# Kernel optimization log

Hardware: AMD Instinct MI355X
Metric: run time of the kernel (lower is better)

## Reference

```python
import jax, jax.numpy as jnp
import numpy as np

N = 50000      # nodes
E = 400000     # directed edges (self-loops added inside reference, per PyG default)
DIN = 256
DH = 32
HEADS = 8
DOUT = 40
SLOPE = 0.2    # GATv2Conv negative_slope default


def _gatv2_layer(x, src, dst, Wl, bl, Wr, br, att, bias, heads, out_ch):
    """One GATv2Conv (concat=True). x:[n,din], src/dst:[e], att:[heads,out_ch]."""
    n = x.shape[0]
    xl = (x @ Wl + bl).reshape(n, heads, out_ch)   # source transform
    xr = (x @ Wr + br).reshape(n, heads, out_ch)   # target transform
    e = jax.nn.leaky_relu(xl[src] + xr[dst], SLOPE)          # [e, H, C]
    s = jnp.einsum('ehc,hc->eh', e, att)                     # per-edge attention logits
    smax = jax.ops.segment_max(s, dst, num_segments=n)       # stable softmax over in-edges
    ex = jnp.exp(s - smax[dst])
    denom = jax.ops.segment_sum(ex, dst, num_segments=n)
    alpha = ex / denom[dst]                                  # [e, H]
    out = jax.ops.segment_sum(alpha[:, :, None] * xl[src], dst, num_segments=n)
    return out.reshape(n, heads * out_ch) + bias


def setup_inputs() -> dict:
    key = jax.random.key(0)
    ks = jax.random.split(key, 8)
    def gl(k, shape, fan_in):
        return jax.random.normal(k, shape, jnp.float32) * np.float32(1.0 / np.sqrt(fan_in))
    return {
        'x': jax.random.normal(ks[0], (N, DIN), jnp.float32),
        'edge_index': jax.random.randint(ks[1], (2, E), 0, N, jnp.int32),
        'W1l': gl(ks[2], (DIN, HEADS * DH), DIN),
        'b1l': jnp.zeros((HEADS * DH,), jnp.float32),
        'W1r': gl(ks[3], (DIN, HEADS * DH), DIN),
        'b1r': jnp.zeros((HEADS * DH,), jnp.float32),
        'att1': gl(ks[4], (HEADS, DH), DH),
        'bias1': jnp.zeros((HEADS * DH,), jnp.float32),
        'W2l': gl(ks[5], (HEADS * DH, DOUT), HEADS * DH),
        'b2l': jnp.zeros((DOUT,), jnp.float32),
        'W2r': gl(ks[6], (HEADS * DH, DOUT), HEADS * DH),
        'b2r': jnp.zeros((DOUT,), jnp.float32),
        'att2': gl(ks[7], (1, DOUT), DOUT),
        'bias2': jnp.zeros((DOUT,), jnp.float32),
    }


def reference(x, edge_index, W1l, b1l, W1r, b1r, att1, bias1,
              W2l, b2l, W2r, b2r, att2, bias2):
    n = x.shape[0]
    loop = jnp.arange(n, dtype=edge_index.dtype)  # add_self_loops=True (PyG default)
    src = jnp.concatenate([edge_index[0], loop])
    dst = jnp.concatenate([edge_index[1], loop])
    # eval mode: F.dropout is identity; normalization='none' -> Identity
    h = _gatv2_layer(x, src, dst, W1l, b1l, W1r, b1r, att1, bias1, HEADS, DH)
    h = jax.nn.elu(h)
    out = _gatv2_layer(h, src, dst, W2l, b2l, W2r, b2r, att2, bias2, 1, DOUT)
    return jax.nn.log_softmax(out, axis=1)
```

## Files before the change

### kernel.cpp

```cpp
#include <hip/hip_runtime.h>
#include <math.h>

#define NODES 50000
#define NEDGE 400000
#define ETOT  450000
#define DIN   256
#define C1    256
#define C2    40
#define SCAN_NB ((NODES + 255) / 256)
#define CSRCAP  600064
#define NB_CNT ((ETOT + 255) / 256)
#define NB_CVT (NODES * DIN / 8 / 256)

typedef __attribute__((ext_vector_type(8))) short bfrag;
typedef __attribute__((ext_vector_type(4))) float facc;

#define GPTR(p) (const __attribute__((address_space(1))) unsigned int*)(p)
#define LPTR(p) (__attribute__((address_space(3))) unsigned int*)(p)

static __device__ __forceinline__ float bitsf(unsigned int x) {
    float f;
    __builtin_memcpy(&f, &x, 4);
    return f;
}
static __device__ __forceinline__ unsigned short f2bf(float f) {
    unsigned int x;
    __builtin_memcpy(&x, &f, 4);
    unsigned int r = x + 0x7fffu + ((x >> 16) & 1u);
    return (unsigned short)(r >> 16);
}
static __device__ __forceinline__ float fexp2(float x) {
#if __has_builtin(__builtin_amdgcn_exp2f)
    return __builtin_amdgcn_exp2f(x);
#else
    return exp2f(x);
#endif
}

__global__ __launch_bounds__(256)
void prep_a(const int* __restrict__ dstRow, int* __restrict__ cnt,
            const float* __restrict__ x, unsigned short* __restrict__ xb)
{
    if (blockIdx.x < NB_CNT) {
        int e = blockIdx.x * 256 + threadIdx.x;
        if (e >= ETOT) return;
        int d = (e < NEDGE) ? dstRow[e] : (e - NEDGE);
        atomicAdd(&cnt[d], 1);
    } else {
        int i = (blockIdx.x - NB_CNT) * 256 + threadIdx.x;
        const float4* p = (const float4*)x + (size_t)i * 2;
        float4 u0 = p[0], u1 = p[1];
        bfrag pk;
        pk[0] = (short)f2bf(u0.x); pk[1] = (short)f2bf(u0.y);
        pk[2] = (short)f2bf(u0.z); pk[3] = (short)f2bf(u0.w);
        pk[4] = (short)f2bf(u1.x); pk[5] = (short)f2bf(u1.y);
        pk[6] = (short)f2bf(u1.z); pk[7] = (short)f2bf(u1.w);
        *(bfrag*)(xb + (size_t)i * 8) = pk;
    }
}

__global__ __launch_bounds__(256)
void prep_ww(const float* __restrict__ W1l, const float* __restrict__ W1r,
             unsigned short* __restrict__ Wt1,
             const float* __restrict__ W2l, const float* __restrict__ W2r,
             unsigned short* __restrict__ Wt2)
{
    if (blockIdx.x < 512) {
        const int idx = blockIdx.x * 256 + threadIdx.x;
        const int n = idx >> 8;
        const int k = idx & 255;
        float v = (n < C1) ? W1l[(size_t)k * C1 + n] : W1r[(size_t)k * C1 + (n - C1)];
        Wt1[idx] = f2bf(v);
    } else {
        const int idx = (blockIdx.x - 512) * 256 + threadIdx.x;
        const int n = idx >> 8;
        const int k = idx & 255;
        if (n >= 2 * C2) return;
        float v = (n < C2) ? W2l[(size_t)k * C2 + n] : W2r[(size_t)k * C2 + (n - C2)];
        Wt2[idx] = f2bf(v);
    }
}

__global__ __launch_bounds__(256)
void scan_blk(const int* __restrict__ cnt, int* __restrict__ off, int* __restrict__ blkTot) {
    __shared__ int buf[256];
    const int t = threadIdx.x;
    const int i = blockIdx.x * 256 + t;
    int v = (i < NODES) ? ((cnt[i] + 3) & ~3) : 0;
    buf[t] = v;
    __syncthreads();
    #pragma unroll
    for (int d = 1; d < 256; d <<= 1) {
        int add = (t >= d) ? buf[t - d] : 0;
        __syncthreads();
        buf[t] += add;
        __syncthreads();
    }
    if (i < NODES) off[i] = buf[t] - v;
    if (t == 255) blkTot[blockIdx.x] = buf[255];
}

__global__ __launch_bounds__(256)
void scan_top(const int* __restrict__ blkTot, int* __restrict__ blkOff, int* __restrict__ offEnd) {
    __shared__ int buf[256];
    const int t = threadIdx.x;
    int v = (t < SCAN_NB) ? blkTot[t] : 0;
    buf[t] = v;
    __syncthreads();
    #pragma unroll
    for (int d = 1; d < 256; d <<= 1) {
        int add = (t >= d) ? buf[t - d] : 0;
        __syncthreads();
        buf[t] += add;
        __syncthreads();
    }
    if (t < SCAN_NB) blkOff[t] = buf[t] - v;
    if (t == 255) *offEnd = buf[255];
}

__global__ __launch_bounds__(256)
void scan_fix(int* __restrict__ off, int* __restrict__ wrk, const int* __restrict__ blkOff) {
    const int i = blockIdx.x * 256 + threadIdx.x;
    if (i < NODES) {
        int v = off[i] + blkOff[blockIdx.x];
        off[i] = v;
        wrk[i] = v;
    }
}

__global__ void place_kernel(const int* __restrict__ srcRow, const int* __restrict__ dstRow,
                             int* __restrict__ wrk, int* __restrict__ csr) {
    int e = blockIdx.x * blockDim.x + threadIdx.x;
    if (e >= ETOT) return;
    int d, s;
    if (e < NEDGE) { d = dstRow[e]; s = srcRow[e]; }
    else           { d = e - NEDGE; s = d; }
    int slot = atomicAdd(&wrk[d], 1);
    csr[slot] = s;
}

#define GBM 128
#define GBN 128
#define GBK 32

template<typename OUTT, bool SWZ>
__global__ __launch_bounds__(256)
void mfma_gemm(const unsigned short* __restrict__ Ab, const unsigned short* __restrict__ Bt,
               const float* __restrict__ bl, const float* __restrict__ br,
               OUTT* __restrict__ Cl, OUTT* __restrict__ Cr,
               int M, int Nrows, int Nhalf, int nbnShift)
{
    __shared__ __align__(16) unsigned short As[3][GBM * GBK];
    __shared__ __align__(16) unsigned short Bs[3][GBN * GBK];

    const int tid  = threadIdx.x;
    const int lane = tid & 63;
    const int w    = tid >> 6;
    const int wr   = w >> 1;
    const int wc   = w & 1;

    int tile;
    if constexpr (SWZ) {
        const int nwg = gridDim.x;
        const int q = nwg >> 3, r = nwg & 7;
        const int xcd = blockIdx.x & 7;
        const int idx = blockIdx.x >> 3;
        tile = (xcd < r ? xcd * (q + 1) : r * (q + 1) + (xcd - r) * q) + idx;
    } else {
        tile = blockIdx.x;
    }
    const int bx   = tile >> nbnShift;
    const int by   = tile & ((1 << nbnShift) - 1);
    const int row0 = bx * GBM;
    const int col0 = by * GBN;

    facc acc[4][4];
    #pragma unroll
    for (int i = 0; i < 4; ++i)
        #pragma unroll
        for (int j = 0; j < 4; ++j) {
            facc z = {0.f, 0.f, 0.f, 0.f};
            acc[i][j] = z;
        }

    const int rA  = lane >> 2;
    const int kgA = (lane & 3) ^ ((rA >> 1) & 3);
    const int fr    = lane & 15;
    const int sRead = (lane >> 4) ^ ((fr >> 1) & 3);

    #define STAGE(bufi, k0)                                                     \
    {                                                                           \
        _Pragma("unroll")                                                       \
        for (int p = 0; p < 2; ++p) {                                           \
            const int chunk = p * 4 + w;                                        \
            const int r_loc = chunk * 16 + rA;                                  \
            const int ga = min(row0 + r_loc, M - 1);                            \
            __builtin_amdgcn_global_load_lds(                                   \
                GPTR(Ab + (size_t)ga * 256 + (k0) + kgA * 8),                   \
                LPTR(&As[bufi][chunk * 512]), 16, 0, 0);                        \
            const int gb = min(col0 + r_loc, Nrows - 1);                        \
            __builtin_amdgcn_global_load_lds(                                   \
                GPTR(Bt + (size_t)gb * 256 + (k0) + kgA * 8),                   \
                LPTR(&Bs[bufi][chunk * 512]), 16, 0, 0);                        \
        }                                                                       \
    }

    #define KSTEP(T, WSTR)                                                      \
    {                                                                           \
        asm volatile("s_waitcnt vmcnt(" WSTR ")" ::: "memory");                 \
        __builtin_amdgcn_s_barrier();                                           \
        __builtin_amdgcn_sched_barrier(0);                                      \
        constexpr int cur = (T) % 3;                                            \
        bfrag af[4], bfv[4];                                                    \
        _Pragma("unroll")                                                       \
        for (int mi = 0; mi < 4; ++mi)                                          \
            af[mi] = *(const bfrag*)(&As[cur][(wr * 64 + mi * 16 + fr) * 32 + sRead * 8]); \
        _Pragma("unroll")                                                       \
        for (int ni = 0; ni < 4; ++ni)                                          \
            bfv[ni] = *(const bfrag*)(&Bs[cur][(wc * 64 + ni * 16 + fr) * 32 + sRead * 8]); \
        if constexpr ((T) + 2 < 8) STAGE(((T) + 2) % 3, ((T) + 2) * GBK);       \
        _Pragma("unroll")                                                       \
        for (int mi = 0; mi < 4; ++mi)                                          \
            _Pragma("unroll")                                                   \
            for (int ni = 0; ni < 4; ++ni)                                      \
                acc[mi][ni] = __builtin_amdgcn_mfma_f32_16x16x32_bf16(          \
                    af[mi], bfv[ni], acc[mi][ni], 0, 0, 0);                     \
    }

    STAGE(0, 0 * GBK);
    STAGE(1, 1 * GBK);
    KSTEP(0, "4"); KSTEP(1, "4"); KSTEP(2, "4"); KSTEP(3, "4");
    KSTEP(4, "4"); KSTEP(5, "4"); KSTEP(6, "4"); KSTEP(7, "0");
    #undef KSTEP
    #undef STAGE

    #pragma unroll
    for (int mi = 0; mi < 4; ++mi) {
        const int rbase = row0 + wr * 64 + mi * 16 + ((lane >> 4) << 2);
        #pragma unroll
        for (int ni = 0; ni < 4; ++ni) {
            const int col = col0 + wc * 64 + ni * 16 + (lane & 15);
            #pragma unroll
            for (int rg = 0; rg < 4; ++rg) {
                int r = rbase + rg;
                if (r >= M) continue;
                float v = acc[mi][ni][rg];
                if (col < Nhalf) {
                    v += bl[col];
                    if constexpr (sizeof(OUTT) == 2)
                        Cl[(size_t)r * Nhalf + col] = (OUTT)f2bf(v);
                    else
                        Cl[(size_t)r * Nhalf + col] = (OUTT)v;
                } else if (col < 2 * Nhalf) {
                    int c2 = col - Nhalf;
                    v += br[c2];
                    if constexpr (sizeof(OUTT) == 2)
                        Cr[(size_t)r * Nhalf + c2] = (OUTT)f2bf(v);
                    else
                        Cr[(size_t)r * Nhalf + c2] = (OUTT)v;
                }
            }
        }
    }
}

__global__ __launch_bounds__(256)
void fused_l1(const int* __restrict__ off, const int* __restrict__ deg,
              const int* __restrict__ csr, const unsigned short* __restrict__ xl,
              const unsigned short* __restrict__ xr, const float* __restrict__ att,
              const float* __restrict__ bias, unsigned short* __restrict__ hout)
{
    const int lane = threadIdx.x & 63;
    const int n    = blockIdx.x * 4 + (threadIdx.x >> 6);
    if (n >= NODES) return;

    const int a  = __builtin_amdgcn_readfirstlane(off[n]);
    const int dn = __builtin_amdgcn_readfirstlane(deg[n]);
    const int np = (dn + 3) & ~3;

    const uint2 xrn = *(const uint2*)(xr + (size_t)n * C1 + lane * 4);
    const float xr0 = bitsf(xrn.x << 16), xr1 = bitsf(xrn.x & 0xffff0000u);
    const float xr2 = bitsf(xrn.y << 16), xr3 = bitsf(xrn.y & 0xffff0000u);
    const float4 wv = *(const float4*)(att + lane * 4);
    const float L2E = 1.4426950408889634f;
    const float w6_0 = wv.x * (0.6f * L2E), w4_0 = wv.x * (0.4f * L2E);
    const float w6_1 = wv.y * (0.6f * L2E), w4_1 = wv.y * (0.4f * L2E);
    const float w6_2 = wv.z * (0.6f * L2E), w4_2 = wv.z * (0.4f * L2E);
    const float w6_3 = wv.w * (0.6f * L2E), w4_3 = wv.w * (0.4f * L2E);

    float m = -INFINITY, d = 0.f;
    float a0 = 0.f, a1 = 0.f, a2 = 0.f, a3 = 0.f;

    uint2 R[4];
    {
        const int4 s4 = *(const int4*)(csr + a);
        R[0] = *(const uint2*)(xl + (size_t)s4.x * C1 + lane * 4);
        R[1] = *(const uint2*)(xl + (size_t)s4.y * C1 + lane * 4);
        R[2] = *(const uint2*)(xl + (size_t)s4.z * C1 + lane * 4);
        R[3] = *(const uint2*)(xl + (size_t)s4.w * C1 + lane * 4);
    }

    for (int i = 0; i < np; i += 4) {
        uint2 Rn[4];
        const int nx = (i + 4 < np) ? (i + 4) : i;
        {
            const int4 s4 = *(const int4*)(csr + a + nx);
            Rn[0] = *(const uint2*)(xl + (size_t)s4.x * C1 + lane * 4);
            Rn[1] = *(const uint2*)(xl + (size_t)s4.y * C1 + lane * 4);
            Rn[2] = *(const uint2*)(xl + (size_t)s4.z * C1 + lane * 4);
            Rn[3] = *(const uint2*)(xl + (size_t)s4.w * C1 + lane * 4);
        }

        float x0[4], x1[4], x2[4], x3[4], p[4];
        #pragma unroll
        for (int k = 0; k < 4; ++k) {
            x0[k] = bitsf(R[k].x << 16);
            x1[k] = bitsf(R[k].x & 0xffff0000u);
            x2[k] = bitsf(R[k].y << 16);
            x3[k] = bitsf(R[k].y & 0xffff0000u);
            const float v0 = x0[k] + xr0, v1 = x1[k] + xr1;
            const float v2 = x2[k] + xr2, v3 = x3[k] + xr3;
            float pp;
            pp = w6_0 * v0;
            pp = fmaf(w4_0, fabsf(v0), pp);
            pp = fmaf(w6_1, v1, pp);
            pp = fmaf(w4_1, fabsf(v1), pp);
            pp = fmaf(w6_2, v2, pp);
            pp = fmaf(w4_2, fabsf(v2), pp);
            pp = fmaf(w6_3, v3, pp);
            pp = fmaf(w4_3, fabsf(v3), pp);
            pp += __shfl_xor(pp, 1);
            pp += __shfl_xor(pp, 2);
            pp += __shfl_xor(pp, 4);
            p[k] = (i + k < dn) ? pp : -INFINITY;
        }

        const float pm = fmaxf(fmaxf(p[0], p[1]), fmaxf(p[2], p[3]));
        if (__any(pm > m + 8.f)) {
            #pragma unroll
            for (int k = 0; k < 4; ++k) {
                const float mN = fmaxf(m, p[k]);
                const float sc = fexp2(m - mN);
                const float wg = fexp2(p[k] - mN);
                m = mN;
                d = fmaf(d, sc, wg);
                a0 = fmaf(wg, x0[k], a0 * sc);
                a1 = fmaf(wg, x1[k], a1 * sc);
                a2 = fmaf(wg, x2[k], a2 * sc);
                a3 = fmaf(wg, x3[k], a3 * sc);
            }
        } else {
            #pragma unroll
            for (int k = 0; k < 4; ++k) {
                const float wg = fexp2(p[k] - m);
                d += wg;
                a0 = fmaf(wg, x0[k], a0);
                a1 = fmaf(wg, x1[k], a1);
                a2 = fmaf(wg, x2[k], a2);
                a3 = fmaf(wg, x3[k], a3);
            }
        }

        #pragma unroll
        for (int k = 0; k < 4; ++k) R[k] = Rn[k];
    }

    const float inv = 1.f / d;
    const float4 bv = *(const float4*)(bias + lane * 4);
    float v0 = fmaf(a0, inv, bv.x), v1 = fmaf(a1, inv, bv.y);
    float v2 = fmaf(a2, inv, bv.z), v3 = fmaf(a3, inv, bv.w);
    v0 = v0 > 0.f ? v0 : (fexp2(v0 * L2E) - 1.f);
    v1 = v1 > 0.f ? v1 : (fexp2(v1 * L2E) - 1.f);
    v2 = v2 > 0.f ? v2 : (fexp2(v2 * L2E) - 1.f);
    v3 = v3 > 0.f ? v3 : (fexp2(v3 * L2E) - 1.f);
    uint2 o;
    o.x = (unsigned int)f2bf(v0) | ((unsigned int)f2bf(v1) << 16);
    o.y = (unsigned int)f2bf(v2) | ((unsigned int)f2bf(v3) << 16);
    *(uint2*)(hout + (size_t)n * C1 + lane * 4) = o;
}

__global__ __launch_bounds__(256)
void fused_l2(const int* __restrict__ off, const int* __restrict__ deg,
              const int* __restrict__ csr, const float* __restrict__ h2l,
              const float* __restrict__ h2r, const float* __restrict__ att,
              const float* __restrict__ bias, float* __restrict__ out)
{
    const int lane = threadIdx.x & 63;
    const int n    = blockIdx.x * 4 + (threadIdx.x >> 6);
    if (n >= NODES) return;
    const int l8 = lane & 7;
    const int g  = lane >> 3;

    const int a  = __builtin_amdgcn_readfirstlane(off[n]);
    const int dn = __builtin_amdgcn_readfirstlane(deg[n]);
    const float L2E = 1.4426950408889634f;

    float w6[5], w4[5], xr[5];
    #pragma unroll
    for (int j = 0; j < 5; ++j) {
        const int c = l8 + 8 * j;
        const float w = att[c];
        w6[j] = w * (0.6f * L2E);
        w4[j] = w * (0.4f * L2E);
        xr[j] = h2r[(size_t)n * C2 + c];
    }

    float m = -INFINITY, dl = 0.f;
    float acc[5] = {0.f, 0.f, 0.f, 0.f, 0.f};

    float R[5];
    {
        const int src = csr[a + g];
        const float* row = h2l + (size_t)src * C2 + l8;
        #pragma unroll
        for (int j = 0; j < 5; ++j) R[j] = row[8 * j];
    }

    for (int c0 = 0; c0 < dn; c0 += 8) {
        float Rn[5];
        {
            const int nx = (c0 + 8 < dn) ? (c0 + 8) : c0;
            const int src = csr[a + nx + g];
            const float* row = h2l + (size_t)src * C2 + l8;
            #pragma unroll
            for (int j = 0; j < 5; ++j) Rn[j] = row[8 * j];
        }

        const int idx = c0 + g;
        float p = 0.f;
        #pragma unroll
        for (int j = 0; j < 5; ++j) {
            const float v = R[j] + xr[j];
            p = fmaf(w6[j], v, p);
            p = fmaf(w4[j], fabsf(v), p);
        }
        p += __shfl_xor(p, 1);
        p += __shfl_xor(p, 2);
        p += __shfl_xor(p, 4);
        if (idx >= dn) p = -INFINITY;

        if (__any(p > m + 8.f)) {
            float pm = p;
            pm = fmaxf(pm, __shfl_xor(pm, 8));
            pm = fmaxf(pm, __shfl_xor(pm, 16));
            pm = fmaxf(pm, __shfl_xor(pm, 32));
            const float mN = fmaxf(m, pm);
            const float sc = fexp2(m - mN);
            const float wg = fexp2(p - mN);
            m = mN;
            dl = fmaf(dl, sc, wg);
            #pragma unroll
            for (int j = 0; j < 5; ++j) acc[j] = fmaf(wg, R[j], acc[j] * sc);
        } else {
            const float wg = fexp2(p - m);
            dl += wg;
            #pragma unroll
            for (int j = 0; j < 5; ++j) acc[j] = fmaf(wg, R[j], acc[j]);
        }

        #pragma unroll
        for (int j = 0; j < 5; ++j) R[j] = Rn[j];
    }

    #pragma unroll
    for (int o = 8; o < 64; o <<= 1) {
        dl += __shfl_xor(dl, o);
        #pragma unroll
        for (int j = 0; j < 5; ++j) acc[j] += __shfl_xor(acc[j], o);
    }

    const float inv = 1.f / dl;
    float v[5];
    float mx = -INFINITY;
    #pragma unroll
    for (int j = 0; j < 5; ++j) {
        v[j] = fmaf(acc[j], inv, bias[l8 + 8 * j]);
        mx = fmaxf(mx, v[j]);
    }
    mx = fmaxf(mx, __shfl_xor(mx, 1));
    mx = fmaxf(mx, __shfl_xor(mx, 2));
    mx = fmaxf(mx, __shfl_xor(mx, 4));
    float s = 0.f;
    #pragma unroll
    for (int j = 0; j < 5; ++j) s += fexp2((v[j] - mx) * L2E);
    s += __shfl_xor(s, 1);
    s += __shfl_xor(s, 2);
    s += __shfl_xor(s, 4);
    const float lg = logf(s);
    if (g == 0) {
        #pragma unroll
        for (int j = 0; j < 5; ++j)
            out[(size_t)n * C2 + l8 + 8 * j] = v[j] - mx - lg;
    }
}

extern "C" void kernel_launch(void* const* d_in, const int* in_sizes, int n_in,
                              void* d_out, int out_size, void* d_ws, size_t ws_size,
                              hipStream_t stream)
{
    const float* x     = (const float*)d_in[0];
    const int*   ei    = (const int*)  d_in[1];
    const float* W1l   = (const float*)d_in[2];
    const float* b1l   = (const float*)d_in[3];
    const float* W1r   = (const float*)d_in[4];
    const float* b1r   = (const float*)d_in[5];
    const float* att1  = (const float*)d_in[6];
    const float* bias1 = (const float*)d_in[7];
    const float* W2l   = (const float*)d_in[8];
    const float* b2l   = (const float*)d_in[9];
    const float* W2r   = (const float*)d_in[10];
    const float* b2r   = (const float*)d_in[11];
    const float* att2  = (const float*)d_in[12];
    const float* bias2 = (const float*)d_in[13];
    float* out = (float*)d_out;

    float* ws = (float*)d_ws;
    unsigned short* xl1 = (unsigned short*)ws;
    unsigned short* xr1 = (unsigned short*)(ws + 6400000);
    unsigned short* xb  = (unsigned short*)(ws + 12800000);
    int*   csr    = (int*)(ws + 19200000);
    int*   off    = csr + CSRCAP;
    int*   cnt    = off + (NODES + 1);
    int*   wrk    = cnt + NODES;
    int*   blkTot = wrk + NODES;
    int*   blkOff = blkTot + SCAN_NB;
    unsigned short* Wt1 = (unsigned short*)(ws + 19960000);
    unsigned short* Wt2 = (unsigned short*)(ws + 20030000);
    unsigned short* h = xr1;
    float* h2l = ws;
    float* h2r = ws + 2000000;

    const int* srcRow = ei;
    const int* dstRow = ei + NEDGE;

    hipMemsetAsync(cnt, 0, NODES * sizeof(int), stream);
    hipMemsetAsync(csr, 0, CSRCAP * sizeof(int), stream);
    prep_a<<<NB_CNT + NB_CVT, 256, 0, stream>>>(dstRow, cnt, x, xb);
    prep_ww<<<512 + 80, 256, 0, stream>>>(W1l, W1r, Wt1, W2l, W2r, Wt2);

    scan_blk<<<SCAN_NB, 256, 0, stream>>>(cnt, off, blkTot);
    scan_top<<<1, 256, 0, stream>>>(blkTot, blkOff, off + NODES);
    scan_fix<<<SCAN_NB, 256, 0, stream>>>(off, wrk, blkOff);
    place_kernel<<<(ETOT + 255) / 256, 256, 0, stream>>>(srcRow, dstRow, wrk, csr);

    mfma_gemm<unsigned short, true><<<((NODES + GBM - 1) / GBM) * 4, 256, 0, stream>>>(
        xb, Wt1, b1l, b1r, xl1, xr1, NODES, 2 * C1, C1, 2);
    fused_l1<<<(NODES + 3) / 4, 256, 0, stream>>>(off, cnt, csr, xl1, xr1, att1, bias1, h);

    mfma_gemm<float, false><<<(NODES + GBM - 1) / GBM, 256, 0, stream>>>(
        h, Wt2, b2l, b2r, h2l, h2r, NODES, 2 * C2, C2, 0);
    fused_l2<<<(NODES + 3) / 4, 256, 0, stream>>>(off, cnt, csr, h2l, h2r, att2, bias2, out);
}
```

Before: 204.3 us.

## Add 128x256-tile, 512-thread GEMM for layer-1 projection with XCD-aware remap

Replaces the generic 128x128 MFMA GEMM for the layer-1 projection (x @ [Wl|Wr]) with a dedicated kernel. It uses 128x256 tiles, 8 waves, double-buffered direct global-to-LDS loads and a fully unrolled K loop. Block indices are remapped so neighbouring tiles land on the same XCD, and larger tiles mean fewer re-reads of the A matrix. The cost is higher LDS and register use per block, which can lower occupancy, and only two buffers are kept where the old kernel used three.

After: 214.4 us. 4.9% more time.

```diff
diff --git a/kernel.cpp b/kernel.cpp
--- a/kernel.cpp
+++ b/kernel.cpp
@@ -137,6 +137,118 @@
     else           { d = e - NEDGE; s = d; }
     int slot = atomicAdd(&wrk[d], 1);
     csr[slot] = s;
+}
+
+__global__ __launch_bounds__(512)
+void gemm1_big(const unsigned short* __restrict__ Ab, const unsigned short* __restrict__ Bt,
+               const float* __restrict__ bl, const float* __restrict__ br,
+               unsigned short* __restrict__ Cl, unsigned short* __restrict__ Cr,
+               int M, int Nhalf)
+{
+    __shared__ __align__(16) unsigned short As[2][128 * 32];
+    __shared__ __align__(16) unsigned short Bs[2][256 * 32];
+
+    const int tid  = threadIdx.x;
+    const int lane = tid & 63;
+    const int w    = tid >> 6;
+    const int wr   = w >> 2;
+    const int wc   = w & 3;
+
+    const int nwg = gridDim.x;
+    const int q = nwg >> 3, r = nwg & 7;
+    const int xcd = blockIdx.x & 7;
+    const int tile = (xcd < r ? xcd * (q + 1) : r * (q + 1) + (xcd - r) * q) + (blockIdx.x >> 3);
+    const int bx   = tile >> 1;
+    const int by   = tile & 1;
+    const int rowB = bx * 128;
+    const int colB = by * 256;
+
+    facc acc[4][4];
+    #pragma unroll
+    for (int i = 0; i < 4; ++i)
+        #pragma unroll
+        for (int j = 0; j < 4; ++j) {
+            facc z = {0.f, 0.f, 0.f, 0.f};
+            acc[i][j] = z;
+        }
+
+    const int rA  = lane >> 2;
+    const int kgA = (lane & 3) ^ ((rA >> 1) & 3);
+    const int fr    = lane & 15;
+    const int sRead = (lane >> 4) ^ ((fr >> 1) & 3);
+
+    #define STAGE(bufi, k0)                                                     \
+    {                                                                           \
+        _Pragma("unroll")                                                       \
+        for (int j = 0; j < 3; ++j) {                                           \
+            const int cid = w * 3 + j;                                          \
+            if (cid < 8) {                                                      \
+                const int r_loc = cid * 16 + rA;                                \
+                const int ga = min(rowB + r_loc, M - 1);                        \
+                __builtin_amdgcn_global_load_lds(                               \
+                    GPTR(Ab + (size_t)ga * 256 + (k0) + kgA * 8),               \
+                    LPTR(&As[bufi][cid * 512]), 16, 0, 0);                      \
+            } else {                                                            \
+                const int c2 = cid - 8;                                         \
+                const int r_loc = c2 * 16 + rA;                                 \
+                const int gb = colB + r_loc;                                    \
+                __builtin_amdgcn_global_load_lds(                               \
+                    GPTR(Bt + (size_t)gb * 256 + (k0) + kgA * 8),               \
+                    LPTR(&Bs[bufi][c2 * 512]), 16, 0, 0);                       \
+            }                                                                   \
+        }                                                                       \
+    }
+
+    #define KSTEP(T, WSTR)                                                      \
+    {                                                                           \
+        if constexpr ((T) + 1 < 8) STAGE(((T) + 1) & 1, ((T) + 1) * 32);        \
+        asm volatile("s_waitcnt vmcnt(" WSTR ")" ::: "memory");                 \
+        __builtin_amdgcn_s_barrier();                                           \
+        __builtin_amdgcn_sched_barrier(0);                                      \
+        constexpr int cur = (T) & 1;                                            \
+        bfrag af[4], bfv[4];                                                    \
+        _Pragma("unroll")                                                       \
+        for (int mi = 0; mi < 4; ++mi)                                          \
+            af[mi] = *(const bfrag*)(&As[cur][(wr * 64 + mi * 16 + fr) * 32 + sRead * 8]); \
+        _Pragma("unroll")                                                       \
+        for (int ni = 0; ni < 4; ++ni)                                          \
+            bfv[ni] = *(const bfrag*)(&Bs[cur][(wc * 64 + ni * 16 + fr) * 32 + sRead * 8]); \
+        _Pragma("unroll")                                                       \
+        for (int mi = 0; mi < 4; ++mi)                                          \
+            _Pragma("unroll")                                                   \
+            for (int ni = 0; ni < 4; ++ni)                                      \
+                acc[mi][ni] = __builtin_amdgcn_mfma_f32_16x16x32_bf16(          \
+                    af[mi], bfv[ni], acc[mi][ni], 0, 0, 0);                     \
+    }
+
+    STAGE(0, 0);
+    KSTEP(0, "3"); KSTEP(1, "3"); KSTEP(2, "3"); KSTEP(3, "3");
+    KSTEP(4, "3"); KSTEP(5, "3"); KSTEP(6, "3"); KSTEP(7, "0");
+    #undef KSTEP
+    #undef STAGE
+
+    #pragma unroll
+    for (int mi = 0; mi < 4; ++mi) {
+        const int rbase = rowB + wr * 64 + mi * 16 + ((lane >> 4) << 2);
+        #pragma unroll
+        for (int ni = 0; ni < 4; ++ni) {
+            const int col = colB + wc * 64 + ni * 16 + fr;
+            #pragma unroll
+            for (int rg = 0; rg < 4; ++rg) {
+                const int rr = rbase + rg;
+                if (rr >= M) continue;
+                float v = acc[mi][ni][rg];
+                if (col < Nhalf) {
+                    v += bl[col];
+                    Cl[(size_t)rr * Nhalf + col] = f2bf(v);
+                } else {
+                    const int c2 = col - Nhalf;
+                    v += br[c2];
+                    Cr[(size_t)rr * Nhalf + c2] = f2bf(v);
+                }
+            }
+        }
+    }
 }
 
 #define GBM 128
@@ -543,8 +655,8 @@
     scan_fix<<<SCAN_NB, 256, 0, stream>>>(off, wrk, blkOff);
     place_kernel<<<(ETOT + 255) / 256, 256, 0, stream>>>(srcRow, dstRow, wrk, csr);
 
-    mfma_gemm<unsigned short, true><<<((NODES + GBM - 1) / GBM) * 4, 256, 0, stream>>>(
-        xb, Wt1, b1l, b1r, xl1, xr1, NODES, 2 * C1, C1, 2);
+    gemm1_big<<<((NODES + 127) / 128) * 2, 512, 0, stream>>>(
+        xb, Wt1, b1l, b1r, xl1, xr1, NODES, C1);
     fused_l1<<<(NODES + 3) / 4, 256, 0, stream>>>(off, cnt, csr, xl1, xr1, att1, bias1, h);
 
     mfma_gemm<float, false><<<(NODES + GBM - 1) / GBM, 256, 0, stream>>>(
```
